# Kernel tuning notes

Measured on AMD Instinct MI355X. Metric: run time of the kernel, lower is better.

The kernel has to match this reference:

```python
import jax, jax.numpy as jnp
import numpy as np

HEADS = 8
DIM_HEAD = 64
NUM_MEM_KV = 4
DIM = 512
B, H, W = 16, 32, 32


def setup_inputs() -> dict:
    key = jax.random.key(0)
    k1, k2, k3, k4 = jax.random.split(key, 4)
    hidden = HEADS * DIM_HEAD
    x = jax.random.normal(k1, (B, DIM, H, W), dtype=jnp.float32)
    gamma = jnp.zeros((DIM,), dtype=jnp.float32)  # nn.Parameter init zeros
    mem_kv = jax.random.normal(k2, (2, HEADS, NUM_MEM_KV, DIM_HEAD), dtype=jnp.float32)
    w_qkv = jax.random.normal(k3, (3 * hidden, DIM), dtype=jnp.float32) * (1.0 / np.sqrt(DIM))
    w_out = jax.random.normal(k4, (DIM, hidden), dtype=jnp.float32) * (1.0 / np.sqrt(hidden))
    return {"x": x, "gamma": gamma, "mem_kv": mem_kv, "w_qkv": w_qkv, "w_out": w_out}


def reference(x, gamma, mem_kv, w_qkv, w_out):
    b, c, h, w = x.shape
    n = h * w
    # RMSNorm: F.normalize over channel dim, then * (gamma+1) * sqrt(dim)
    denom = jnp.maximum(jnp.linalg.norm(x, axis=1, keepdims=True), 1e-12)
    xn = (x / denom) * (gamma[None, :, None, None] + 1.0) * (c ** 0.5)
    # 1x1 conv qkv projection
    qkv = jnp.einsum('bchw,oc->bohw', xn, w_qkv)  # [b, 3*hidden, h, w]
    q, k, v = jnp.split(qkv, 3, axis=1)

    def to_heads(t):
        # 'b (h c) x y -> b h (x y) c'
        return t.reshape(b, HEADS, DIM_HEAD, n).transpose(0, 1, 3, 2)

    q = to_heads(q) * (DIM_HEAD ** -0.5)  # [b, heads, n, d]
    k = to_heads(k)
    v = to_heads(v)
    mk = jnp.broadcast_to(mem_kv[0], (b, HEADS, NUM_MEM_KV, DIM_HEAD))
    mv = jnp.broadcast_to(mem_kv[1], (b, HEADS, NUM_MEM_KV, DIM_HEAD))
    k = jnp.concatenate([mk, k], axis=2)  # [b, heads, m+n, d]
    v = jnp.concatenate([mv, v], axis=2)
    sim = jnp.einsum('bhid,bhjd->bhij', q, k)
    attn = jax.nn.softmax(sim, axis=-1)
    out = jnp.einsum('bhij,bhjd->bhid', attn, v)  # [b, heads, n, d]
    # 'b h (x y) d -> b (h d) x y'
    out = out.transpose(0, 1, 3, 2).reshape(b, HEADS * DIM_HEAD, h, w)
    return jnp.einsum('bchw,oc->bohw', out, w_out)
```

## Files before the change

kernel.cpp:

```cpp
#include <hip/hip_runtime.h>
#include <cstdint>
#include <cstddef>

constexpr int kHeads = 8;
constexpr int kDHead = 64;
constexpr int kC     = 512;
constexpr int kB     = 16;
constexpr int kN     = 1024;
constexpr int kHid   = 512;

typedef _Float16 h16;
typedef _Float16 h8 __attribute__((ext_vector_type(8)));
typedef _Float16 h4 __attribute__((ext_vector_type(4)));
typedef float f32x4 __attribute__((ext_vector_type(4)));

__global__ __launch_bounds__(256) void rms_transpose_kernel(
    const float* __restrict__ x, h16* __restrict__ xh)
{
  __shared__ float T[64 * 64];
  __shared__ float red[4][64];
  __shared__ float sl[64];
  const int t  = threadIdx.x;
  const int b  = blockIdx.x >> 4;
  const int p0 = (blockIdx.x & 15) << 6;
  const float* xb = x + (size_t)b * kC * kN + p0;

  const int pix = t & 63, sub = t >> 6;
  float sum = 0.f;
  #pragma unroll 8
  for (int c = sub * 128; c < sub * 128 + 128; ++c) {
    const float v = xb[(size_t)c * kN + pix];
    sum = fmaf(v, v, sum);
  }
  red[sub][pix] = sum;
  __syncthreads();
  if (t < 64) {
    const float tot = red[0][t] + red[1][t] + red[2][t] + red[3][t];
    sl[t] = 22.62741699796952f / fmaxf(sqrtf(tot), 1e-12f);
  }
  __syncthreads();

  for (int cc = 0; cc < 8; cc++) {
    const int c0 = cc * 64;
    #pragma unroll
    for (int i = 0; i < 4; i++) {
      const int r  = i * 16 + (t >> 4);
      const int pg = t & 15;
      const float4 v = *(const float4*)(xb + (size_t)(c0 + r) * kN + pg * 4);
      *(float4*)&T[r * 64 + ((pg ^ (r & 15)) << 2)] = v;
    }
    __syncthreads();
    #pragma unroll
    for (int i2 = 0; i2 < 2; i2++) {
      const int p  = i2 * 32 + (t >> 3);
      const int cg = t & 7;
      const float sc = sl[p];
      h16 hv[8];
      #pragma unroll
      for (int j = 0; j < 8; j++) {
        const int c = cg * 8 + j;
        const float v = T[c * 64 + (((p >> 2) ^ (c & 15)) << 2) + (p & 3)];
        hv[j] = (h16)(v * sc);
      }
      *(h8*)&xh[((size_t)b * kN + p0 + p) * kC + c0 + cg * 8] = *(h8*)hv;
    }
    __syncthreads();
  }
}

__global__ __launch_bounds__(64) void prep_w_kernel(
    const float* __restrict__ w_qkv, const float* __restrict__ gamma,
    const float* __restrict__ w_out, h16* __restrict__ wqh,
    h16* __restrict__ wouth)
{
  const int row = blockIdx.x;
  const int c0  = threadIdx.x * 8;
  if (row < 1536) {
    const float sc = (row < 512) ? 0.125f : 1.f;
    const float4 a  = *(const float4*)(w_qkv + (size_t)row * kC + c0);
    const float4 b  = *(const float4*)(w_qkv + (size_t)row * kC + c0 + 4);
    const float4 g0 = *(const float4*)(gamma + c0);
    const float4 g1 = *(const float4*)(gamma + c0 + 4);
    h8 hv = { (h16)(a.x * (g0.x + 1.f) * sc), (h16)(a.y * (g0.y + 1.f) * sc),
              (h16)(a.z * (g0.z + 1.f) * sc), (h16)(a.w * (g0.w + 1.f) * sc),
              (h16)(b.x * (g1.x + 1.f) * sc), (h16)(b.y * (g1.y + 1.f) * sc),
              (h16)(b.z * (g1.z + 1.f) * sc), (h16)(b.w * (g1.w + 1.f) * sc) };
    *(h8*)&wqh[(size_t)row * kC + c0] = hv;
  } else {
    const int r = row - 1536;
    const float4 a = *(const float4*)(w_out + (size_t)r * kC + c0);
    const float4 b = *(const float4*)(w_out + (size_t)r * kC + c0 + 4);
    h8 hv = { (h16)a.x, (h16)a.y, (h16)a.z, (h16)a.w,
              (h16)b.x, (h16)b.y, (h16)b.z, (h16)b.w };
    *(h8*)&wouth[(size_t)r * kC + c0] = hv;
  }
}

__device__ __forceinline__ void gemm_loop_f16(
    const h16* __restrict__ Ag, const h16* __restrict__ Bg,
    h16 (*__restrict__ As)[8192], h16 (*__restrict__ Bs)[8192],
    int t, int w, int g, int lo, f32x4 (&acc)[4][4])
{
  const int wo = (w >> 1) * 64, wp = (w & 1) * 64;
  h8 stA[4], stB[4];
  auto load = [&](int kt) {
    const int k0 = kt * 64;
    #pragma unroll
    for (int i = 0; i < 4; i++) {
      const int f = t + i * 256, r = f >> 3, cg = f & 7;
      stA[i] = *(const h8*)(Ag + (size_t)r * kC + k0 + cg * 8);
      stB[i] = *(const h8*)(Bg + (size_t)r * kC + k0 + cg * 8);
    }
  };
  auto store = [&](int buf) {
    #pragma unroll
    for (int i = 0; i < 4; i++) {
      const int f = t + i * 256, r = f >> 3, cg = f & 7;
      const int off = r * 64 + ((cg ^ (r & 7)) << 3);
      *(h8*)&As[buf][off] = stA[i];
      *(h8*)&Bs[buf][off] = stB[i];
    }
  };
  load(0); store(0); __syncthreads();
  int buf = 0;
  for (int kt = 0; kt < 8; kt++) {
    if (kt < 7) load(kt + 1);
    h8 bfr[4][2];
    #pragma unroll
    for (int ni = 0; ni < 4; ni++) {
      const int row = wp + ni * 16 + lo;
      #pragma unroll
      for (int kb = 0; kb < 2; kb++)
        bfr[ni][kb] = *(const h8*)&Bs[buf][row * 64 + (((kb * 4 + g) ^ (row & 7)) << 3)];
    }
    #pragma unroll
    for (int mi = 0; mi < 4; mi++) {
      const int row = wo + mi * 16 + lo;
      const h8 a0 = *(const h8*)&As[buf][row * 64 + (((    g) ^ (row & 7)) << 3)];
      const h8 a1 = *(const h8*)&As[buf][row * 64 + (((4 + g) ^ (row & 7)) << 3)];
      #pragma unroll
      for (int ni = 0; ni < 4; ni++) {
        acc[mi][ni] = __builtin_amdgcn_mfma_f32_16x16x32_f16(a0, bfr[ni][0], acc[mi][ni], 0, 0, 0);
        acc[mi][ni] = __builtin_amdgcn_mfma_f32_16x16x32_f16(a1, bfr[ni][1], acc[mi][ni], 0, 0, 0);
      }
    }
    if (kt < 7) store(buf ^ 1);
    __syncthreads();
    buf ^= 1;
  }
}

__global__ __launch_bounds__(256) void qkv_mfma_kernel(
    const h16* __restrict__ xh, const h16* __restrict__ wqh,
    h16* __restrict__ Qh, h16* __restrict__ Kh, h16* __restrict__ VTh)
{
  __shared__ h16 As[2][8192];
  __shared__ h16 Bs[2][8192];
  const int t = threadIdx.x, lane = t & 63, w = t >> 6, g = lane >> 4, lo = lane & 15;
  const int o0 = blockIdx.x * 128;
  const int p0 = blockIdx.y * 128;
  const int b  = blockIdx.z;
  const h16* Ag = wqh + (size_t)o0 * kC;
  const h16* Bg = xh + ((size_t)b * kN + p0) * kC;

  f32x4 acc[4][4];
  #pragma unroll
  for (int mi = 0; mi < 4; mi++)
    #pragma unroll
    for (int ni = 0; ni < 4; ni++) { f32x4 z = {0.f, 0.f, 0.f, 0.f}; acc[mi][ni] = z; }

  gemm_loop_f16(Ag, Bg, As, Bs, t, w, g, lo, acc);

  const int o_wave = o0 + (w >> 1) * 64;
  const int which  = o_wave >> 9;
  const int head   = (o_wave >> 6) & 7;
  const size_t bh  = (size_t)b * kHeads + head;
  const int pglob  = p0 + (w & 1) * 64;

  if (which == 2) {
    h16* Vdst = VTh + bh * (size_t)(kN * kDHead);
    #pragma unroll
    for (int mi = 0; mi < 4; mi++)
      #pragma unroll
      for (int ni = 0; ni < 4; ni++) {
        const int p = pglob + ni * 16 + lo;
        #pragma unroll
        for (int r = 0; r < 4; r++) {
          const int d = mi * 16 + g * 4 + r;
          Vdst[(size_t)d * kN + p] = (h16)((const float*)&acc[mi][ni])[r];
        }
      }
  } else {
    h16* lw = &As[0][0] + w * 4096;
    #pragma unroll
    for (int mi = 0; mi < 4; mi++) {
      const int gran0 = mi * 2 + (g >> 1);
      const int off   = (g & 1) * 4;
      #pragma unroll
      for (int ni = 0; ni < 4; ni++) {
        const int p = ni * 16 + lo;
        h4 pv = { (h16)acc[mi][ni].x, (h16)acc[mi][ni].y,
                  (h16)acc[mi][ni].z, (h16)acc[mi][ni].w };
        *(h4*)&lw[p * 64 + ((gran0 ^ (p & 7)) << 3) + off] = pv;
      }
    }
    __syncthreads();
    h16* dst = (which ? Kh : Qh) + bh * (size_t)(kN * kDHead);
    #pragma unroll
    for (int i = 0; i < 8; i++) {
      const int p  = i * 8 + (lane >> 3);
      const int dg = lane & 7;
      const h8 v = *(const h8*)&lw[p * 64 + ((dg ^ (p & 7)) << 3)];
      *(h8*)&dst[((size_t)pglob + p) * kDHead + dg * 8] = v;
    }
  }
}

__global__ __launch_bounds__(256, 2) void attn_mfma_kernel(
    const h16* __restrict__ Qh, const h16* __restrict__ Kh,
    const h16* __restrict__ VTh, const float* __restrict__ mem_kv,
    h16* __restrict__ ah)
{
  __shared__ h16 Kl[2][4096];
  __shared__ h16 Vl[2][4096];
  __shared__ h16 Pl[4][4096];

  const int t    = threadIdx.x;
  const int lane = t & 63;
  const int w    = t >> 6;
  const int g    = lane >> 4;
  const int lo   = lane & 15;
  const int qt = blockIdx.x, h = blockIdx.y, b = blockIdx.z;
  const size_t bh = (size_t)b * kHeads + h;

  const h16* Qg = Qh  + bh * 65536;
  const h16* Kg = Kh  + bh * 65536;
  const h16* Vg = VTh + bh * 65536;
  const int q0 = qt * 256 + w * 64;

  h8 qf[4][2];
  #pragma unroll
  for (int ni = 0; ni < 4; ni++)
    #pragma unroll
    for (int kb = 0; kb < 2; kb++)
      qf[ni][kb] = *(const h8*)(Qg + (size_t)(q0 + ni*16 + lo) * 64 + kb*32 + g*8);

  {
    const int kr = t >> 2, dq = (t & 3) << 4;
    h16 hv[16];
    if (kr < 4) {
      const float* src = mem_kv + (size_t)h * 256 + kr * 64 + dq;
      #pragma unroll
      for (int i = 0; i < 16; i++) hv[i] = (h16)src[i];
    } else {
      #pragma unroll
      for (int i = 0; i < 16; i++) hv[i] = (h16)0.f;
    }
    const int sw = (kr & 7) << 3;
    *(h8*)&Kl[0][kr*64 + ( dq      ^ sw)] = *(h8*)&hv[0];
    *(h8*)&Kl[0][kr*64 + ((dq + 8) ^ sw)] = *(h8*)&hv[8];

    const int d = t >> 2, kq = (t & 3) << 4;
    h16 vv[16];
    #pragma unroll
    for (int i = 0; i < 16; i++) vv[i] = (h16)0.f;
    if (kq == 0) {
      const float* src = mem_kv + 2048 + (size_t)h * 256 + d;
      #pragma unroll
      for (int i = 0; i < 4; i++) vv[i] = (h16)src[i * 64];
    }
    const int sv = (d & 7) << 3;
    *(h8*)&Vl[0][d*64 + ( kq      ^ sv)] = *(h8*)&vv[0];
    *(h8*)&Vl[0][d*64 + ((kq + 8) ^ sv)] = *(h8*)&vv[8];
  }
  __syncthreads();

  f32x4 o[4][4];
  #pragma unroll
  for (int mi = 0; mi < 4; mi++)
    #pragma unroll
    for (int ni = 0; ni < 4; ni++) { f32x4 z = {0.f,0.f,0.f,0.f}; o[mi][ni] = z; }
  float mst[4] = {-1e30f, -1e30f, -1e30f, -1e30f};
  float lst[4] = {0.f, 0.f, 0.f, 0.f};

  int cur = 0;
  h8 stK[2], stV[2];
  for (int kt = 0; kt <= 16; kt++) {
    if (kt < 16) {
      const size_t key0 = (size_t)kt * 64;
      #pragma unroll
      for (int ps = 0; ps < 2; ps++) {
        const int f = t + ps*256, r = f >> 3, cb = (f & 7) << 3;
        stK[ps] = *(const h8*)(Kg + (key0 + r) * 64 + cb);
        stV[ps] = *(const h8*)(Vg + (size_t)r * 1024 + key0 + cb);
      }
    }
    const h16* KL = Kl[cur];
    const h16* VL = Vl[cur];
    h16* PL = Pl[w];

    f32x4 s[4][4];
    #pragma unroll
    for (int mi = 0; mi < 4; mi++) {
      const int row = mi*16 + lo;
      const int sw = (row & 7) << 3;
      const h8 k0 = *(const h8*)&KL[row*64 + (( g*8)      ^ sw)];
      const h8 k1 = *(const h8*)&KL[row*64 + ((32 + g*8)  ^ sw)];
      #pragma unroll
      for (int ni = 0; ni < 4; ni++) {
        f32x4 acc = {0.f, 0.f, 0.f, 0.f};
        acc = __builtin_amdgcn_mfma_f32_16x16x32_f16(k0, qf[ni][0], acc, 0, 0, 0);
        acc = __builtin_amdgcn_mfma_f32_16x16x32_f16(k1, qf[ni][1], acc, 0, 0, 0);
        s[mi][ni] = acc;
      }
    }
    if (kt == 0) {
      const f32x4 neg = {-1e30f, -1e30f, -1e30f, -1e30f};
      #pragma unroll
      for (int ni = 0; ni < 4; ni++) {
        #pragma unroll
        for (int mi = 1; mi < 4; mi++) s[mi][ni] = neg;
        if (g > 0) s[0][ni] = neg;
      }
    }

    float sc[4];
    #pragma unroll
    for (int ni = 0; ni < 4; ni++) {
      float m0 = fmaxf(fmaxf(s[0][ni].x, s[0][ni].y), fmaxf(s[0][ni].z, s[0][ni].w));
      #pragma unroll
      for (int mi = 1; mi < 4; mi++)
        m0 = fmaxf(m0, fmaxf(fmaxf(s[mi][ni].x, s[mi][ni].y), fmaxf(s[mi][ni].z, s[mi][ni].w)));
      m0 = fmaxf(m0, __shfl_xor(m0, 16));
      m0 = fmaxf(m0, __shfl_xor(m0, 32));
      const float mn = fmaxf(mst[ni], m0);
      sc[ni] = __expf(mst[ni] - mn);
      mst[ni] = mn;
      float rs = 0.f;
      #pragma unroll
      for (int mi = 0; mi < 4; mi++) {
        f32x4 p;
        p.x = __expf(s[mi][ni].x - mn);
        p.y = __expf(s[mi][ni].y - mn);
        p.z = __expf(s[mi][ni].z - mn);
        p.w = __expf(s[mi][ni].w - mn);
        s[mi][ni] = p;
        rs += p.x + p.y + p.z + p.w;
      }
      rs += __shfl_xor(rs, 16);
      rs += __shfl_xor(rs, 32);
      lst[ni] = lst[ni] * sc[ni] + rs;
    }

    #pragma unroll
    for (int ni = 0; ni < 4; ni++) {
      const int row = ni*16 + lo;
      const int swp = (row & 7) << 3;
      #pragma unroll
      for (int mi = 0; mi < 4; mi++) {
        h4 pv = { (h16)s[mi][ni].x, (h16)s[mi][ni].y, (h16)s[mi][ni].z, (h16)s[mi][ni].w };
        *(h4*)&PL[row*64 + ((mi*16 + g*4) ^ swp)] = pv;
      }
    }

    #pragma unroll
    for (int mi = 0; mi < 4; mi++) {
      const float r0 = __shfl(sc[mi], g*4 + 0);
      const float r1 = __shfl(sc[mi], g*4 + 1);
      const float r2 = __shfl(sc[mi], g*4 + 2);
      const float r3 = __shfl(sc[mi], g*4 + 3);
      #pragma unroll
      for (int ni = 0; ni < 4; ni++) {
        o[mi][ni].x *= r0; o[mi][ni].y *= r1;
        o[mi][ni].z *= r2; o[mi][ni].w *= r3;
      }
    }

    h8 vf[2][4];
    #pragma unroll
    for (int ni = 0; ni < 4; ni++) {
      const int row = ni*16 + lo;
      const int swv = (row & 7) << 3;
      vf[0][ni] = *(const h8*)&VL[row*64 + (( g*8)     ^ swv)];
      vf[1][ni] = *(const h8*)&VL[row*64 + ((32 + g*8) ^ swv)];
    }
    #pragma unroll
    for (int mi = 0; mi < 4; mi++) {
      const int row = mi*16 + lo;
      const int swp = (row & 7) << 3;
      const h8 p0 = *(const h8*)&PL[row*64 + (( g*8)     ^ swp)];
      const h8 p1 = *(const h8*)&PL[row*64 + ((32 + g*8) ^ swp)];
      #pragma unroll
      for (int ni = 0; ni < 4; ni++) {
        o[mi][ni] = __builtin_amdgcn_mfma_f32_16x16x32_f16(p0, vf[0][ni], o[mi][ni], 0, 0, 0);
        o[mi][ni] = __builtin_amdgcn_mfma_f32_16x16x32_f16(p1, vf[1][ni], o[mi][ni], 0, 0, 0);
      }
    }

    if (kt < 16) {
      #pragma unroll
      for (int ps = 0; ps < 2; ps++) {
        const int f = t + ps*256, r = f >> 3, cb = (f & 7) << 3;
        const int sw = (r & 7) << 3;
        *(h8*)&Kl[cur ^ 1][r*64 + (cb ^ sw)] = stK[ps];
        *(h8*)&Vl[cur ^ 1][r*64 + (cb ^ sw)] = stV[ps];
      }
    }
    __syncthreads();
    cur ^= 1;
  }

  #pragma unroll
  for (int mi = 0; mi < 4; mi++) {
    const float il = 1.f / lst[mi];
    const float i0 = __shfl(il, g*4 + 0);
    const float i1 = __shfl(il, g*4 + 1);
    const float i2 = __shfl(il, g*4 + 2);
    const float i3 = __shfl(il, g*4 + 3);
    const int qg = (b << 10) + q0 + mi*16 + g*4;
    #pragma unroll
    for (int ni = 0; ni < 4; ni++) {
      const int c = h*64 + ni*16 + lo;
      ah[(size_t)(qg + 0) * kHid + c] = (h16)(o[mi][ni].x * i0);
      ah[(size_t)(qg + 1) * kHid + c] = (h16)(o[mi][ni].y * i1);
      ah[(size_t)(qg + 2) * kHid + c] = (h16)(o[mi][ni].z * i2);
      ah[(size_t)(qg + 3) * kHid + c] = (h16)(o[mi][ni].w * i3);
    }
  }
}

__global__ __launch_bounds__(256) void out_mfma_kernel(
    const h16* __restrict__ ah, const h16* __restrict__ wouth,
    float* __restrict__ out)
{
  __shared__ h16 As[2][8192];
  __shared__ h16 Bs[2][8192];
  const int t = threadIdx.x, lane = t & 63, w = t >> 6, g = lane >> 4, lo = lane & 15;
  const int o0 = blockIdx.x * 128;
  const int p0 = blockIdx.y * 128;
  const int b  = blockIdx.z;
  const h16* Ag = wouth + (size_t)o0 * kC;
  const h16* Bg = ah + ((size_t)b * kN + p0) * kC;

  f32x4 acc[4][4];
  #pragma unroll
  for (int mi = 0; mi < 4; mi++)
    #pragma unroll
    for (int ni = 0; ni < 4; ni++) { f32x4 z = {0.f, 0.f, 0.f, 0.f}; acc[mi][ni] = z; }

  gemm_loop_f16(Ag, Bg, As, Bs, t, w, g, lo, acc);

  const int ow = o0 + (w >> 1) * 64;
  const int pw = p0 + (w & 1) * 64;
  #pragma unroll
  for (int mi = 0; mi < 4; mi++)
    #pragma unroll
    for (int ni = 0; ni < 4; ni++) {
      const int p = pw + ni * 16 + lo;
      #pragma unroll
      for (int r = 0; r < 4; r++) {
        const int o = ow + mi * 16 + g * 4 + r;
        out[((size_t)b * kHid + o) * kN + p] = ((const float*)&acc[mi][ni])[r];
      }
    }
}

extern "C" void kernel_launch(void* const* d_in, const int* in_sizes, int n_in,
                              void* d_out, int out_size, void* d_ws, size_t ws_size,
                              hipStream_t stream) {
  (void)in_sizes; (void)n_in; (void)out_size; (void)ws_size;
  const float* x      = (const float*)d_in[0];
  const float* gamma  = (const float*)d_in[1];
  const float* mem_kv = (const float*)d_in[2];
  const float* w_qkv  = (const float*)d_in[3];
  const float* w_out  = (const float*)d_in[4];
  float* out = (float*)d_out;

  h16* xh    = (h16*)d_ws;
  h16* Qh    = xh + (size_t)16777216;
  h16* Kh    = Qh + (size_t)8388608;
  h16* VTh   = Kh + (size_t)8388608;
  h16* ah    = VTh + (size_t)8388608;
  h16* wqh   = ah + (size_t)8388608;
  h16* wouth = wqh + (size_t)786432;

  rms_transpose_kernel<<<256, 256, 0, stream>>>(x, xh);
  prep_w_kernel<<<2048, 64, 0, stream>>>(w_qkv, gamma, w_out, wqh, wouth);
  qkv_mfma_kernel<<<dim3(12, 8, 16), 256, 0, stream>>>(xh, wqh, Qh, Kh, VTh);
  attn_mfma_kernel<<<dim3(4, 8, 16), 256, 0, stream>>>(Qh, Kh, VTh, mem_kv, ah);
  out_mfma_kernel<<<dim3(4, 8, 16), 256, 0, stream>>>(ah, wouth, out);
}
```

Measured before the change: 151.4 us.

## Keep softmax probabilities in registers and use lazy rescaling in attention

The attention kernel stops writing P to shared memory and reads it back. It keeps P in registers as 16x16x16 MFMA operands and reads V in a matching layout. The Q weights are pre-scaled by log2(e) so exp2f replaces __expf. The running max is only rescaled when the tile max exceeds it by a threshold (FA4-style lazy rescale). It also raises occupancy to 3 blocks per SM, swizzles the block index for XCD locality, and adds setprio around the MFMA sections. Risks: higher register pressure under the tighter launch bound, and fp16 overflow headroom from the lazy rescale.

```diff
diff --git a/kernel.cpp b/kernel.cpp
--- a/kernel.cpp
+++ b/kernel.cpp
@@ -76,7 +76,7 @@
   const int row = blockIdx.x;
   const int c0  = threadIdx.x * 8;
   if (row < 1536) {
-    const float sc = (row < 512) ? 0.125f : 1.f;
+    const float sc = (row < 512) ? 0.125f * 1.4426950408889634f : 1.f;
     const float4 a  = *(const float4*)(w_qkv + (size_t)row * kC + c0);
     const float4 b  = *(const float4*)(w_qkv + (size_t)row * kC + c0 + 4);
     const float4 g0 = *(const float4*)(gamma + c0);
@@ -216,21 +216,22 @@
   }
 }
 
-__global__ __launch_bounds__(256, 2) void attn_mfma_kernel(
+__global__ __launch_bounds__(256, 3) void attn_mfma_kernel(
     const h16* __restrict__ Qh, const h16* __restrict__ Kh,
     const h16* __restrict__ VTh, const float* __restrict__ mem_kv,
     h16* __restrict__ ah)
 {
   __shared__ h16 Kl[2][4096];
   __shared__ h16 Vl[2][4096];
-  __shared__ h16 Pl[4][4096];
 
   const int t    = threadIdx.x;
   const int lane = t & 63;
   const int w    = t >> 6;
   const int g    = lane >> 4;
   const int lo   = lane & 15;
-  const int qt = blockIdx.x, h = blockIdx.y, b = blockIdx.z;
+  const int id  = blockIdx.x;
+  const int swz = (id & 7) * 64 + (id >> 3);
+  const int qt = swz & 3, h = (swz >> 2) & 7, b = swz >> 5;
   const size_t bh = (size_t)b * kHeads + h;
 
   const h16* Qg = Qh  + bh * 65536;
@@ -277,9 +278,9 @@
 
   f32x4 o[4][4];
   #pragma unroll
-  for (int mi = 0; mi < 4; mi++)
-    #pragma unroll
-    for (int ni = 0; ni < 4; ni++) { f32x4 z = {0.f,0.f,0.f,0.f}; o[mi][ni] = z; }
+  for (int qb = 0; qb < 4; qb++)
+    #pragma unroll
+    for (int db = 0; db < 4; db++) { f32x4 z = {0.f,0.f,0.f,0.f}; o[qb][db] = z; }
   float mst[4] = {-1e30f, -1e30f, -1e30f, -1e30f};
   float lst[4] = {0.f, 0.f, 0.f, 0.f};
 
@@ -297,9 +298,9 @@
     }
     const h16* KL = Kl[cur];
     const h16* VL = Vl[cur];
-    h16* PL = Pl[w];
 
     f32x4 s[4][4];
+    __builtin_amdgcn_s_setprio(1);
     #pragma unroll
     for (int mi = 0; mi < 4; mi++) {
       const int row = mi*16 + lo;
@@ -314,6 +315,7 @@
         s[mi][ni] = acc;
       }
     }
+    __builtin_amdgcn_s_setprio(0);
     if (kt == 0) {
       const f32x4 neg = {-1e30f, -1e30f, -1e30f, -1e30f};
       #pragma unroll
@@ -324,7 +326,7 @@
       }
     }
 
-    float sc[4];
+    float tm[4];
     #pragma unroll
     for (int ni = 0; ni < 4; ni++) {
       float m0 = fmaxf(fmaxf(s[0][ni].x, s[0][ni].y), fmaxf(s[0][ni].z, s[0][ni].w));
@@ -333,69 +335,72 @@
         m0 = fmaxf(m0, fmaxf(fmaxf(s[mi][ni].x, s[mi][ni].y), fmaxf(s[mi][ni].z, s[mi][ni].w)));
       m0 = fmaxf(m0, __shfl_xor(m0, 16));
       m0 = fmaxf(m0, __shfl_xor(m0, 32));
-      const float mn = fmaxf(mst[ni], m0);
-      sc[ni] = __expf(mst[ni] - mn);
-      mst[ni] = mn;
+      tm[ni] = m0;
+    }
+
+    const bool need = (tm[0] > mst[0] + 11.f) || (tm[1] > mst[1] + 11.f) ||
+                      (tm[2] > mst[2] + 11.f) || (tm[3] > mst[3] + 11.f);
+    if (__any(need)) {
+      float sc[4];
+      #pragma unroll
+      for (int ni = 0; ni < 4; ni++) {
+        const float mn = fmaxf(mst[ni], tm[ni]);
+        sc[ni] = exp2f(mst[ni] - mn);
+        mst[ni] = mn;
+        lst[ni] *= sc[ni];
+      }
+      #pragma unroll
+      for (int qb = 0; qb < 4; qb++) {
+        const float r0 = __shfl(sc[qb], g*4 + 0);
+        const float r1 = __shfl(sc[qb], g*4 + 1);
+        const float r2 = __shfl(sc[qb], g*4 + 2);
+        const float r3 = __shfl(sc[qb], g*4 + 3);
+        #pragma unroll
+        for (int db = 0; db < 4; db++) {
+          o[qb][db].x *= r0; o[qb][db].y *= r1;
+          o[qb][db].z *= r2; o[qb][db].w *= r3;
+        }
+      }
+    }
+
+    h4 p4[4][4];
+    #pragma unroll
+    for (int ni = 0; ni < 4; ni++) {
       float rs = 0.f;
       #pragma unroll
       for (int mi = 0; mi < 4; mi++) {
         f32x4 p;
-        p.x = __expf(s[mi][ni].x - mn);
-        p.y = __expf(s[mi][ni].y - mn);
-        p.z = __expf(s[mi][ni].z - mn);
-        p.w = __expf(s[mi][ni].w - mn);
-        s[mi][ni] = p;
+        p.x = exp2f(s[mi][ni].x - mst[ni]);
+        p.y = exp2f(s[mi][ni].y - mst[ni]);
+        p.z = exp2f(s[mi][ni].z - mst[ni]);
+        p.w = exp2f(s[mi][ni].w - mst[ni]);
         rs += p.x + p.y + p.z + p.w;
+        h4 pv = { (h16)p.x, (h16)p.y, (h16)p.z, (h16)p.w };
+        p4[mi][ni] = pv;
       }
       rs += __shfl_xor(rs, 16);
       rs += __shfl_xor(rs, 32);
-      lst[ni] = lst[ni] * sc[ni] + rs;
-    }
-
-    #pragma unroll
-    for (int ni = 0; ni < 4; ni++) {
-      const int row = ni*16 + lo;
-      const int swp = (row & 7) << 3;
-      #pragma unroll
-      for (int mi = 0; mi < 4; mi++) {
-        h4 pv = { (h16)s[mi][ni].x, (h16)s[mi][ni].y, (h16)s[mi][ni].z, (h16)s[mi][ni].w };
-        *(h4*)&PL[row*64 + ((mi*16 + g*4) ^ swp)] = pv;
-      }
-    }
-
-    #pragma unroll
-    for (int mi = 0; mi < 4; mi++) {
-      const float r0 = __shfl(sc[mi], g*4 + 0);
-      const float r1 = __shfl(sc[mi], g*4 + 1);
-      const float r2 = __shfl(sc[mi], g*4 + 2);
-      const float r3 = __shfl(sc[mi], g*4 + 3);
-      #pragma unroll
-      for (int ni = 0; ni < 4; ni++) {
-        o[mi][ni].x *= r0; o[mi][ni].y *= r1;
-        o[mi][ni].z *= r2; o[mi][ni].w *= r3;
-      }
-    }
-
-    h8 vf[2][4];
-    #pragma unroll
-    for (int ni = 0; ni < 4; ni++) {
-      const int row = ni*16 + lo;
-      const int swv = (row & 7) << 3;
-      vf[0][ni] = *(const h8*)&VL[row*64 + (( g*8)     ^ swv)];
-      vf[1][ni] = *(const h8*)&VL[row*64 + ((32 + g*8) ^ swv)];
-    }
-    #pragma unroll
-    for (int mi = 0; mi < 4; mi++) {
-      const int row = mi*16 + lo;
-      const int swp = (row & 7) << 3;
-      const h8 p0 = *(const h8*)&PL[row*64 + (( g*8)     ^ swp)];
-      const h8 p1 = *(const h8*)&PL[row*64 + ((32 + g*8) ^ swp)];
-      #pragma unroll
-      for (int ni = 0; ni < 4; ni++) {
-        o[mi][ni] = __builtin_amdgcn_mfma_f32_16x16x32_f16(p0, vf[0][ni], o[mi][ni], 0, 0, 0);
-        o[mi][ni] = __builtin_amdgcn_mfma_f32_16x16x32_f16(p1, vf[1][ni], o[mi][ni], 0, 0, 0);
-      }
-    }
+      lst[ni] += rs;
+    }
+
+    h4 v4[4][4];
+    #pragma unroll
+    for (int db = 0; db < 4; db++) {
+      const int d = db*16 + lo;
+      const int sw = (d & 7) << 3;
+      #pragma unroll
+      for (int mi = 0; mi < 4; mi++)
+        v4[mi][db] = *(const h4*)&VL[d*64 + ((mi*16 + (g>>1)*8) ^ sw) + (g&1)*4];
+    }
+    __builtin_amdgcn_s_setprio(1);
+    #pragma unroll
+    for (int qb = 0; qb < 4; qb++)
+      #pragma unroll
+      for (int db = 0; db < 4; db++)
+        #pragma unroll
+        for (int mi = 0; mi < 4; mi++)
+          o[qb][db] = __builtin_amdgcn_mfma_f32_16x16x16f16(p4[mi][qb], v4[mi][db], o[qb][db], 0, 0, 0);
+    __builtin_amdgcn_s_setprio(0);
 
     if (kt < 16) {
       #pragma unroll
@@ -411,20 +416,20 @@
   }
 
   #pragma unroll
-  for (int mi = 0; mi < 4; mi++) {
-    const float il = 1.f / lst[mi];
+  for (int qb = 0; qb < 4; qb++) {
+    const float il = 1.f / lst[qb];
     const float i0 = __shfl(il, g*4 + 0);
     const float i1 = __shfl(il, g*4 + 1);
     const float i2 = __shfl(il, g*4 + 2);
     const float i3 = __shfl(il, g*4 + 3);
-    const int qg = (b << 10) + q0 + mi*16 + g*4;
-    #pragma unroll
-    for (int ni = 0; ni < 4; ni++) {
-      const int c = h*64 + ni*16 + lo;
-      ah[(size_t)(qg + 0) * kHid + c] = (h16)(o[mi][ni].x * i0);
-      ah[(size_t)(qg + 1) * kHid + c] = (h16)(o[mi][ni].y * i1);
-      ah[(size_t)(qg + 2) * kHid + c] = (h16)(o[mi][ni].z * i2);
-      ah[(size_t)(qg + 3) * kHid + c] = (h16)(o[mi][ni].w * i3);
+    const int qg = (b << 10) + q0 + qb*16 + g*4;
+    #pragma unroll
+    for (int db = 0; db < 4; db++) {
+      const int c = h*64 + db*16 + lo;
+      ah[(size_t)(qg + 0) * kHid + c] = (h16)(o[qb][db].x * i0);
+      ah[(size_t)(qg + 1) * kHid + c] = (h16)(o[qb][db].y * i1);
+      ah[(size_t)(qg + 2) * kHid + c] = (h16)(o[qb][db].z * i2);
+      ah[(size_t)(qg + 3) * kHid + c] = (h16)(o[qb][db].w * i3);
     }
   }
 }
@@ -459,8 +464,8 @@
       const int p = pw + ni * 16 + lo;
       #pragma unroll
       for (int r = 0; r < 4; r++) {
-        const int o = ow + mi * 16 + g * 4 + r;
-        out[((size_t)b * kHid + o) * kN + p] = ((const float*)&acc[mi][ni])[r];
+        const int oc = ow + mi * 16 + g * 4 + r;
+        out[((size_t)b * kHid + oc) * kN + p] = ((const float*)&acc[mi][ni])[r];
       }
     }
 }
@@ -487,6 +492,6 @@
   rms_transpose_kernel<<<256, 256, 0, stream>>>(x, xh);
   prep_w_kernel<<<2048, 64, 0, stream>>>(w_qkv, gamma, w_out, wqh, wouth);
   qkv_mfma_kernel<<<dim3(12, 8, 16), 256, 0, stream>>>(xh, wqh, Qh, Kh, VTh);
-  attn_mfma_kernel<<<dim3(4, 8, 16), 256, 0, stream>>>(Qh, Kh, VTh, mem_kv, ah);
+  attn_mfma_kernel<<<512, 256, 0, stream>>>(Qh, Kh, VTh, mem_kv, ah);
   out_mfma_kernel<<<dim3(4, 8, 16), 256, 0, stream>>>(ah, wouth, out);
 }
```

Measured after the change: 283.0 us. 86.9% more time.
